# Performance work log

Hardware: AMD Instinct MI355X
Metric: run time of the kernel (lower is better)

## Reference

```python
import jax, jax.numpy as jnp
import numpy as np
from jax.scipy.special import logsumexp

V, C, S, H = 32000, 4096, 32, 512
B, T = 32, 256
NEG = jnp.float32(-1e10)  # masked_fill value used by mask_emission


def _res(x, w1, b1, w2, b2):
    # ResidualLayerOld: relu(lin1(x)); relu(lin2(h) + x)
    h = jax.nn.relu(x @ w1.T + b1)
    return jax.nn.relu(h @ w2.T + b2 + x)


def setup_inputs() -> dict:
    key = jax.random.key(0)
    ks = jax.random.split(key, 16)
    g = lambda i, shape, s=0.02: jax.random.normal(ks[i], shape, jnp.float32) * s
    return {
        "text": jax.random.randint(ks[0], (B, T), 0, V),
        "word2state": jax.random.randint(ks[1], (V, S), 0, C - 1),
        "start_emb": g(2, (C, H), 1.0),
        "start_w1": g(3, (H, H)), "start_b1": jnp.zeros((H,), jnp.float32),
        "start_w2": g(4, (H, H)), "start_b2": jnp.zeros((H,), jnp.float32),
        "start_w3": g(5, (1, H)), "start_b3": jnp.zeros((1,), jnp.float32),
        "state_emb": g(6, (C, H), 1.0),
        "trans_w1": g(7, (H, H)), "trans_b1": jnp.zeros((H,), jnp.float32),
        "trans_w2": g(8, (H, H)), "trans_b2": jnp.zeros((H,), jnp.float32),
        "next_state_proj": g(9, (C, H)),
        "preterminal_emb": g(10, (C, H), 1.0),
        "term_w1": g(11, (H, H)), "term_b1": jnp.zeros((H,), jnp.float32),
        "term_w2": g(12, (H, H)), "term_b2": jnp.zeros((H,), jnp.float32),
        "term_w3": g(13, (V, H)), "term_b3": jnp.zeros((V,), jnp.float32),
    }


def _forward(text, word2state, start_emb, start_w1, start_b1, start_w2, start_b2,
             start_w3, start_b3, state_emb, trans_w1, trans_b1, trans_w2, trans_b2,
             next_state_proj, preterminal_emb, term_w1, term_b1, term_w2, term_b2,
             term_w3, term_b3):
    ninf = -jnp.inf
    # start distribution over states [C]
    start = jax.nn.log_softmax(
        (_res(start_emb, start_w1, start_b1, start_w2, start_b2) @ start_w3.T + start_b3)[:, 0])
    # transition [C, C]: mask last column, row-normalize, mask last row (pad state)
    tl = _res(state_emb, trans_w1, trans_b1, trans_w2, trans_b2) @ next_state_proj.T
    tl = tl.at[:, -1].set(ninf)
    trans = jax.nn.log_softmax(tl, axis=-1)
    trans = jnp.where(jnp.isnan(trans), ninf, trans)
    trans = trans.at[-1, :].set(ninf)
    # emission [C, V]: sparse word2state mask, normalize over vocab
    el = _res(preterminal_emb, term_w1, term_b1, term_w2, term_b2) @ term_w3.T + term_b3
    emask = jnp.zeros((C, V), bool).at[
        word2state.reshape(-1), jnp.repeat(jnp.arange(V), S)].set(True)
    emit = jax.nn.log_softmax(jnp.where(emask, el, NEG), axis=-1)
    emit = jnp.where(jnp.isnan(emit), ninf, emit)
    emit = emit.at[-1, :].set(ninf)
    # clamp to the S states allowed for each observed word
    cs = word2state[text]                                  # [B, T, S]
    pot = trans[cs[:, :-1, :, None], cs[:, 1:, None, :]]   # [B, T-1, S, S] (cur, next)
    obs = emit[cs, text[:, :, None]]                       # [B, T, S]
    init = start[cs[:, 0]]                                 # [B, S]
    pot = pot + obs[:, 1:, None, :]                        # obs at t+1 on next axis
    pot = pot.at[:, 0].add(init[:, :, None] + obs[:, 0, :, None])
    pot = jnp.swapaxes(pot, -1, -2)                        # [B, T-1, next, prev]
    # log-domain forward scan (the fb kernel's alpha recursion)
    alpha0 = logsumexp(pot[:, 0], axis=-1)                 # [B, S]
    def step(alpha, p):
        return logsumexp(p + alpha[:, None, :], axis=-1), None
    alpha, _ = jax.lax.scan(step, alpha0, jnp.swapaxes(pot[:, 1:], 0, 1))
    return logsumexp(alpha, axis=-1).sum()                 # evidence (sum over batch)


def reference(text, word2state, start_emb, start_w1, start_b1, start_w2, start_b2,
              start_w3, start_b3, state_emb, trans_w1, trans_b1, trans_w2, trans_b2,
              next_state_proj, preterminal_emb, term_w1, term_b1, term_w2, term_b2,
              term_w3, term_b3):
    return _forward(text, word2state, start_emb, start_w1, start_b1, start_w2,
                    start_b2, start_w3, start_b3, state_emb, trans_w1, trans_b1,
                    trans_w2, trans_b2, next_state_proj, preterminal_emb, term_w1,
                    term_b1, term_w2, term_b2, term_w3, term_b3)
```

## Files before the change

### kernel.cpp

```cpp
#include <hip/hip_runtime.h>
#include <hip/hip_bf16.h>
#include <math.h>

#define NV 32000
#define NC 4096
#define NS 32
#define NH 512
#define NB 32
#define NT 256

typedef short s16x8 __attribute__((ext_vector_type(8)));
typedef float f32x4 __attribute__((ext_vector_type(4)));

__device__ __forceinline__ float wredMax(float v){
  #pragma unroll
  for (int o = 32; o; o >>= 1) v = fmaxf(v, __shfl_xor(v, o, 64));
  return v;
}
__device__ __forceinline__ float wredSum(float v){
  #pragma unroll
  for (int o = 32; o; o >>= 1) v += __shfl_xor(v, o, 64);
  return v;
}
__device__ __forceinline__ int f2ord(float f){ int i = __float_as_int(f); return i >= 0 ? i : (i ^ 0x7fffffff); }
__device__ __forceinline__ float ord2f(int i){ return __int_as_float(i >= 0 ? i : (i ^ 0x7fffffff)); }

__device__ __forceinline__ unsigned short f2bf(float x){
  unsigned int u = __float_as_uint(x);
  return (unsigned short)((u + 0x7fffu + ((u >> 16) & 1u)) >> 16);
}
__device__ __forceinline__ float bf2f(unsigned short h){
  return __uint_as_float((unsigned int)h << 16);
}

__device__ __forceinline__ void conv_body(const float* __restrict__ src,
                                          unsigned short* __restrict__ dst, int idx)
{
  const float* s = src + (size_t)idx * 8;
  float4 f0 = *(const float4*)s;
  float4 f1 = *(const float4*)(s + 4);
  float fv[8] = {f0.x, f0.y, f0.z, f0.w, f1.x, f1.y, f1.z, f1.w};
  s16x8 vh, vl;
  #pragma unroll
  for (int e = 0; e < 8; ++e) {
    unsigned short h = f2bf(fv[e]);
    vh[e] = (short)h;
    vl[e] = (short)f2bf(fv[e] - bf2f(h));
  }
  int r = idx >> 6, c8 = idx & 63;
  unsigned short* d = dst + (size_t)r * 1024 + c8 * 8;
  *(s16x8*)d = vh;
  *(s16x8*)(d + 512) = vl;
}

struct ConvArgs {
  const float* src[10];
  unsigned short* dst[10];
  int rows[10];
};

__global__ __launch_bounds__(256)
void conv_batch(ConvArgs a)
{
  int z = blockIdx.y;
  int idx = blockIdx.x * 256 + threadIdx.x;
  if (idx >= a.rows[z] * 64) return;
  conv_body(a.src[z], a.dst[z], idx);
}

template<int BM>
__global__ __launch_bounds__(256)
void gemm_bf16s(const unsigned short* __restrict__ Asp, const unsigned short* __restrict__ Bsp,
                float* __restrict__ Co, int M, int N, int K)
{
  constexpr int BN = 128;
  constexpr int MF = BM / 32;
  constexpr int NFR = 4;
  __shared__ char smem[BM * 128 + BN * 128];
  char* smA = smem;
  char* smB = smem + BM * 128;

  const int tid  = threadIdx.x;
  const int lane = tid & 63, w = tid >> 6;
  const int wr = w >> 1, wc = w & 1;
  const int bm = blockIdx.y * BM, bn = blockIdx.x * BN;
  const int lda = 2 * K;
  const int l8 = lane >> 3, s8 = lane & 7;
  const int frow = lane & 15, kgrp = lane >> 4;

  f32x4 acc[MF][NFR] = {};

  #pragma unroll 1
  for (int seg = 0; seg < 3; ++seg) {
    const int aoff = (seg == 1) ? K : 0;
    const int boff = (seg == 2) ? K : 0;
    #pragma unroll 1
    for (int k0 = 0; k0 < K; k0 += 64) {
      #pragma unroll
      for (int c = 0; c < MF; ++c) {
        int q = w * MF + c;
        int row = q * 8 + l8;
        s16x8 v = *(const s16x8*)(Asp + (size_t)(bm + row) * lda + aoff + k0 + s8 * 8);
        unsigned int o = (unsigned int)(row * 128 + (s8 << 4));
        o ^= (unsigned int)((row & 7) << 4);
        *(s16x8*)(smA + o) = v;
      }
      #pragma unroll
      for (int c = 0; c < NFR; ++c) {
        int q = w * NFR + c;
        int row = q * 8 + l8;
        s16x8 v = *(const s16x8*)(Bsp + (size_t)(bn + row) * lda + boff + k0 + s8 * 8);
        unsigned int o = (unsigned int)(row * 128 + (s8 << 4));
        o ^= (unsigned int)((row & 7) << 4);
        *(s16x8*)(smB + o) = v;
      }
      __syncthreads();
      #pragma unroll
      for (int kk = 0; kk < 64; kk += 32) {
        s16x8 af[MF], bfr[NFR];
        #pragma unroll
        for (int im = 0; im < MF; ++im) {
          int ar = wr * (BM / 2) + im * 16 + frow;
          unsigned int o = ((unsigned int)(ar * 128 + (kk + kgrp * 8) * 2)) ^ ((unsigned int)((ar & 7) << 4));
          af[im] = *(const s16x8*)(smA + o);
        }
        #pragma unroll
        for (int jn = 0; jn < NFR; ++jn) {
          int bc = wc * 64 + jn * 16 + frow;
          unsigned int o = ((unsigned int)(bc * 128 + (kk + kgrp * 8) * 2)) ^ ((unsigned int)((bc & 7) << 4));
          bfr[jn] = *(const s16x8*)(smB + o);
        }
        #pragma unroll
        for (int im = 0; im < MF; ++im)
          #pragma unroll
          for (int jn = 0; jn < NFR; ++jn)
            asm volatile("v_mfma_f32_16x16x32_bf16 %0, %1, %2, %0"
                         : "+v"(acc[im][jn]) : "v"(af[im]), "v"(bfr[jn]));
      }
      __syncthreads();
    }
  }
  asm volatile("s_nop 7\n\ts_nop 7" ::: );
  #pragma unroll
  for (int im = 0; im < MF; ++im) {
    int row0 = bm + wr * (BM / 2) + im * 16 + kgrp * 4;
    #pragma unroll
    for (int jn = 0; jn < NFR; ++jn) {
      int col = bn + wc * 64 + jn * 16 + frow;
      #pragma unroll
      for (int j = 0; j < 4; ++j)
        Co[(size_t)(row0 + j) * N + col] = acc[im][jn][j];
    }
  }
}

struct G3 {
  const unsigned short* A[3];
  const unsigned short* B[3];
  const float* bias[3];
  const float* res[3];
  float* Cf[3];
  unsigned short* Cs[3];
};

template<bool RES>
__global__ __launch_bounds__(256)
void gemm3(G3 a)
{
  constexpr int BM = 64, BN = 128, K = 512, N = 512;
  constexpr int MF = 2, NFR = 4;
  __shared__ char smem[BM * 128 + BN * 128];
  char* smA = smem;
  char* smB = smem + BM * 128;

  const int z = blockIdx.z;
  const unsigned short* Asp = a.A[z];
  const unsigned short* Bsp = a.B[z];
  const float* bias = a.bias[z];
  float* Cf = a.Cf[z];
  unsigned short* Cs = a.Cs[z];

  const int tid  = threadIdx.x;
  const int lane = tid & 63, w = tid >> 6;
  const int wr = w >> 1, wc = w & 1;
  const int bm = blockIdx.y * BM, bn = blockIdx.x * BN;
  const int lda = 2 * K;
  const int l8 = lane >> 3, s8 = lane & 7;
  const int frow = lane & 15, kgrp = lane >> 4;

  f32x4 acc[MF][NFR] = {};

  #pragma unroll 1
  for (int seg = 0; seg < 3; ++seg) {
    const int aoff = (seg == 1) ? K : 0;
    const int boff = (seg == 2) ? K : 0;
    #pragma unroll 1
    for (int k0 = 0; k0 < K; k0 += 64) {
      #pragma unroll
      for (int c = 0; c < MF; ++c) {
        int q = w * MF + c;
        int row = q * 8 + l8;
        s16x8 v = *(const s16x8*)(Asp + (size_t)(bm + row) * lda + aoff + k0 + s8 * 8);
        unsigned int o = (unsigned int)(row * 128 + (s8 << 4));
        o ^= (unsigned int)((row & 7) << 4);
        *(s16x8*)(smA + o) = v;
      }
      #pragma unroll
      for (int c = 0; c < NFR; ++c) {
        int q = w * NFR + c;
        int row = q * 8 + l8;
        s16x8 v = *(const s16x8*)(Bsp + (size_t)(bn + row) * lda + boff + k0 + s8 * 8);
        unsigned int o = (unsigned int)(row * 128 + (s8 << 4));
        o ^= (unsigned int)((row & 7) << 4);
        *(s16x8*)(smB + o) = v;
      }
      __syncthreads();
      #pragma unroll
      for (int kk = 0; kk < 64; kk += 32) {
        s16x8 af[MF], bfr[NFR];
        #pragma unroll
        for (int im = 0; im < MF; ++im) {
          int ar = wr * (BM / 2) + im * 16 + frow;
          unsigned int o = ((unsigned int)(ar * 128 + (kk + kgrp * 8) * 2)) ^ ((unsigned int)((ar & 7) << 4));
          af[im] = *(const s16x8*)(smA + o);
        }
        #pragma unroll
        for (int jn = 0; jn < NFR; ++jn) {
          int bc = wc * 64 + jn * 16 + frow;
          unsigned int o = ((unsigned int)(bc * 128 + (kk + kgrp * 8) * 2)) ^ ((unsigned int)((bc & 7) << 4));
          bfr[jn] = *(const s16x8*)(smB + o);
        }
        #pragma unroll
        for (int im = 0; im < MF; ++im)
          #pragma unroll
          for (int jn = 0; jn < NFR; ++jn)
            asm volatile("v_mfma_f32_16x16x32_bf16 %0, %1, %2, %0"
                         : "+v"(acc[im][jn]) : "v"(af[im]), "v"(bfr[jn]));
      }
      __syncthreads();
    }
  }
  asm volatile("s_nop 7\n\ts_nop 7" ::: );
  #pragma unroll
  for (int im = 0; im < MF; ++im) {
    int row0 = bm + wr * (BM / 2) + im * 16 + kgrp * 4;
    #pragma unroll
    for (int jn = 0; jn < NFR; ++jn) {
      int col = bn + wc * 64 + jn * 16 + frow;
      #pragma unroll
      for (int j = 0; j < 4; ++j) {
        int r = row0 + j;
        float v = acc[im][jn][j] + bias[col];
        if constexpr (RES) v += a.res[z][(size_t)r * N + col];
        v = fmaxf(v, 0.f);
        if (Cf) Cf[(size_t)r * N + col] = v;
        if (Cs) {
          unsigned short hi = f2bf(v);
          Cs[(size_t)r * 1024 + col] = hi;
          Cs[(size_t)r * 1024 + 512 + col] = f2bf(v - bf2f(hi));
        }
      }
    }
  }
}

__global__ __launch_bounds__(64)
void dot_head(const float* __restrict__ hS, const float* __restrict__ w3,
              const float* __restrict__ b3, float* __restrict__ sv)
{
  int c = blockIdx.x, lane = threadIdx.x;
  const float* hrow = hS + (size_t)c * NH;
  float acc = 0.f;
  #pragma unroll
  for (int e = 0; e < 8; ++e) acc += hrow[lane + e*64] * w3[lane + e*64];
  acc = wredSum(acc);
  if (lane == 0) sv[c] = acc + b3[0];
}

__global__ __launch_bounds__(1024)
void lse_vec(const float* __restrict__ x, int n, float* __restrict__ out)
{
  int tid = threadIdx.x;
  __shared__ float sm[16], ss[16];
  float m = -INFINITY;
  for (int i = tid; i < n; i += 1024) m = fmaxf(m, x[i]);
  m = wredMax(m);
  if ((tid & 63) == 0) sm[tid >> 6] = m;
  __syncthreads();
  m = sm[0];
  #pragma unroll
  for (int wv = 1; wv < 16; ++wv) m = fmaxf(m, sm[wv]);
  float s = 0.f;
  for (int i = tid; i < n; i += 1024) s += expf(x[i] - m);
  s = wredSum(s);
  if ((tid & 63) == 0) ss[tid >> 6] = s;
  __syncthreads();
  if (tid == 0) {
    float tot = 0.f;
    #pragma unroll
    for (int wv = 0; wv < 16; ++wv) tot += ss[wv];
    out[0] = m + logf(tot);
  }
}

__global__ __launch_bounds__(256)
void row_lse_trans(const float* __restrict__ tl, float* __restrict__ lse_t)
{
  int c = blockIdx.x;
  const float* row = tl + (size_t)c * NC;
  int tid = threadIdx.x;
  __shared__ float sm[4], ss[4];
  float m = -INFINITY;
  for (int n = tid; n < NC - 1; n += 256) m = fmaxf(m, row[n]);
  m = wredMax(m);
  if ((tid & 63) == 0) sm[tid >> 6] = m;
  __syncthreads();
  m = fmaxf(fmaxf(sm[0], sm[1]), fmaxf(sm[2], sm[3]));
  float s = 0.f;
  for (int n = tid; n < NC - 1; n += 256) s += expf(row[n] - m);
  s = wredSum(s);
  if ((tid & 63) == 0) ss[tid >> 6] = s;
  __syncthreads();
  if (tid == 0) lse_t[c] = m + logf(ss[0] + ss[1] + ss[2] + ss[3]);
}

__global__ __launch_bounds__(256)
void el_kernel(const int* __restrict__ w2s, const float* __restrict__ hP,
               const float* __restrict__ w3, const float* __restrict__ b3,
               float* __restrict__ el_g, unsigned int* __restrict__ vmask)
{
  int v = blockIdx.x;
  __shared__ float w3v[NH];
  __shared__ int crow[NS];
  int tid = threadIdx.x;
  if (tid < NS) crow[tid] = w2s[(size_t)v * NS + tid];
  for (int e = tid; e < NH; e += 256) w3v[e] = w3[(size_t)v * NH + e];
  __syncthreads();
  if (tid < 64) {
    bool valid = false;
    if (tid < NS) {
      valid = true;
      int c = crow[tid];
      for (int s2 = 0; s2 < tid; ++s2) if (crow[s2] == c) { valid = false; break; }
    }
    unsigned long long bal = __ballot(valid);
    if (tid == 0) vmask[v] = (unsigned int)(bal & 0xffffffffull);
  }
  int wave = tid >> 6, lane = tid & 63;
  float b3v = b3[v];
  #pragma unroll
  for (int q = 0; q < 8; ++q) {
    int s = wave * 8 + q;
    int c = crow[s];
    const float* hrow = hP + (size_t)c * NH;
    float acc = 0.f;
    #pragma unroll
    for (int e = 0; e < 8; ++e) acc += hrow[lane + e*64] * w3v[lane + e*64];
    acc = wredSum(acc);
    if (lane == 0) el_g[(size_t)v * NS + s] = acc + b3v;
  }
}

__global__ __launch_bounds__(256)
void init_e(int* __restrict__ emax, unsigned long long* __restrict__ esum)
{
  int i = blockIdx.x * 256 + threadIdx.x;
  if (i < NC) { emax[i] = 0x80000000; esum[i] = 0ull; }
}
__global__ __launch_bounds__(256)
void emit_max_k(const int* __restrict__ w2s, const float* __restrict__ el_g,
                const unsigned int* __restrict__ vmask, int* __restrict__ emax)
{
  int idx = blockIdx.x * 256 + threadIdx.x;
  int v = idx >> 5, s = idx & 31;
  if (!((vmask[v] >> s) & 1u)) return;
  atomicMax(&emax[w2s[idx]], f2ord(el_g[idx]));
}
__global__ __launch_bounds__(256)
void emit_sum_k(const int* __restrict__ w2s, const float* __restrict__ el_g,
                const unsigned int* __restrict__ vmask, const int* __restrict__ emax,
                unsigned long long* __restrict__ esum)
{
  int idx = blockIdx.x * 256 + threadIdx.x;
  int v = idx >> 5, s = idx & 31;
  if (!((vmask[v] >> s) & 1u)) return;
  int c = w2s[idx];
  float p = expf(el_g[idx] - ord2f(emax[c]));
  atomicAdd(&esum[c], (unsigned long long)(p * 0x1p40f));
}
__global__ __launch_bounds__(256)
void emit_fin_k(const int* __restrict__ emax, const unsigned long long* __restrict__ esum,
                float* __restrict__ lse_e)
{
  int c = blockIdx.x * 256 + threadIdx.x;
  if (c < NC) lse_e[c] = ord2f(emax[c]) + logf((float)esum[c] * 0x1p-40f);
}

__global__ __launch_bounds__(256)
void build_D(const int* __restrict__ text, const int* __restrict__ w2s,
             const float* __restrict__ el_g, const float* __restrict__ lse_e,
             const float* __restrict__ lse_t, const float* __restrict__ sv,
             const float* __restrict__ lse_s,
             float* __restrict__ Dall, float* __restrict__ Dlast,
             float* __restrict__ beta0, unsigned short* __restrict__ cs_all)
{
  int idx = blockIdx.x * 256 + threadIdx.x;
  int s = idx & 31;
  int bt = idx >> 5;
  int t = bt & (NT - 1);
  int b = bt >> 8;
  int v = text[bt];
  int c = w2s[(size_t)v * NS + s];
  cs_all[idx] = (unsigned short)c;
  float D = el_g[(size_t)v * NS + s] - lse_e[c] - lse_t[c];
  Dall[idx] = D;
  if (t == NT - 1) Dlast[b * NS + s] = D + lse_t[c];
  if (t == 0)      beta0[b * NS + s] = sv[c] - lse_s[0] + D;
}

__global__ __launch_bounds__(1024)
void gather_pot(const unsigned short* __restrict__ cs_all, const float* __restrict__ tl,
                float* __restrict__ pot)
{
  int t = blockIdx.x;
  int b = blockIdx.y;
  int tid = threadIdx.x;
  __shared__ unsigned short c1s[NS], c2s[NS];
  if (tid < NS) c1s[tid] = cs_all[((size_t)b * NT + t) * NS + tid];
  else if (tid < 2 * NS) c2s[tid - NS] = cs_all[((size_t)b * NT + t + 1) * NS + (tid - NS)];
  __syncthreads();
  int gi = tid >> 5, gj = tid & 31;
  float v = tl[(size_t)c1s[gi] * NC + c2s[gj]];
  pot[((size_t)b * (NT - 1) + t) * 1024 + gj * 32 + gi] = v;
}

__device__ __forceinline__ float lse_step(float4 p0, float4 p1, float4 p2, float4 p3,
                                          float beta, int h16)
{
  float pv[16] = {p0.x,p0.y,p0.z,p0.w, p1.x,p1.y,p1.z,p1.w,
                  p2.x,p2.y,p2.z,p2.w, p3.x,p3.y,p3.z,p3.w};
  float xs[16];
  #pragma unroll
  for (int q = 0; q < 16; ++q)
    xs[q] = pv[q] + __shfl(beta, h16 + q, 64);
  float a[8];
  #pragma unroll
  for (int q = 0; q < 8; ++q) a[q] = fmaxf(xs[q], xs[q + 8]);
  float c4[4];
  #pragma unroll
  for (int q = 0; q < 4; ++q) c4[q] = fmaxf(a[q], a[q + 4]);
  float m = fmaxf(fmaxf(c4[0], c4[1]), fmaxf(c4[2], c4[3]));
  m = fmaxf(m, __shfl_xor(m, 32, 64));
  float e[8];
  #pragma unroll
  for (int q = 0; q < 8; ++q) e[q] = __expf(xs[q] - m) + __expf(xs[q + 8] - m);
  float s4[4];
  #pragma unroll
  for (int q = 0; q < 4; ++q) s4[q] = e[q] + e[q + 4];
  float st = (s4[0] + s4[1]) + (s4[2] + s4[3]);
  st += __shfl_xor(st, 32, 64);
  return m + __logf(st);
}

__global__ __launch_bounds__(64)
void scan_kernel(const float* __restrict__ pot, const float* __restrict__ Dall,
                 const float* __restrict__ Dlast, const float* __restrict__ beta0,
                 float* __restrict__ out_b)
{
  const int b = blockIdx.x;
  const int lane = threadIdx.x;
  const int j = lane & 31;
  const int h16 = (lane >> 5) * 16;
  const float* potb = pot + (size_t)b * (NT - 1) * 1024 + j * 32 + h16;
  const float* Db = Dall + (size_t)b * NT * NS + j;

  float beta = beta0[b * NS + j];

  float4 A0 = *(const float4*)(potb + 0);
  float4 A1 = *(const float4*)(potb + 4);
  float4 A2 = *(const float4*)(potb + 8);
  float4 A3 = *(const float4*)(potb + 12);
  const float* pB0 = potb + 1024;
  float4 B0 = *(const float4*)(pB0 + 0);
  float4 B1 = *(const float4*)(pB0 + 4);
  float4 B2 = *(const float4*)(pB0 + 8);
  float4 B3 = *(const float4*)(pB0 + 12);
  float dA = Db[1 * NS];
  float dB = Db[2 * NS];

  #pragma unroll 1
  for (int t = 0; t < NT - 2; t += 2) {
    float r = lse_step(A0, A1, A2, A3, beta, h16);
    beta = r + dA;
    const float* pn = potb + (size_t)(t + 2) * 1024;
    A0 = *(const float4*)(pn + 0);
    A1 = *(const float4*)(pn + 4);
    A2 = *(const float4*)(pn + 8);
    A3 = *(const float4*)(pn + 12);
    dA = Db[(t + 3 < NT ? t + 3 : NT - 1) * NS];
    float r2 = lse_step(B0, B1, B2, B3, beta, h16);
    beta = r2 + dB;
    int tb = (t + 3 < NT - 1) ? t + 3 : NT - 2;
    const float* pn2 = potb + (size_t)tb * 1024;
    B0 = *(const float4*)(pn2 + 0);
    B1 = *(const float4*)(pn2 + 4);
    B2 = *(const float4*)(pn2 + 8);
    B3 = *(const float4*)(pn2 + 12);
    dB = Db[(t + 4 < NT ? t + 4 : NT - 1) * NS];
  }
  float r = lse_step(A0, A1, A2, A3, beta, h16);
  float rfin = r + Dlast[b * NS + j];

  float m = rfin;
  #pragma unroll
  for (int o = 16; o; o >>= 1) m = fmaxf(m, __shfl_xor(m, o, 32));
  float p = expf(rfin - m);
  #pragma unroll
  for (int o = 16; o; o >>= 1) p += __shfl_xor(p, o, 32);
  if (lane == 0) out_b[b] = m + logf(p);
}

__global__ void final_sum(const float* __restrict__ out_b, float* __restrict__ out)
{
  if (threadIdx.x == 0) {
    float s = 0.f;
    for (int b = 0; b < NB; ++b) s += out_b[b];
    out[0] = s;
  }
}

extern "C" void kernel_launch(void* const* d_in, const int* in_sizes, int n_in,
                              void* d_out, int out_size, void* d_ws, size_t ws_size,
                              hipStream_t stream)
{
  (void)in_sizes; (void)n_in; (void)out_size; (void)ws_size;
  const int*   text      = (const int*)d_in[0];
  const int*   w2s       = (const int*)d_in[1];
  const float* start_emb = (const float*)d_in[2];
  const float* start_w1  = (const float*)d_in[3];
  const float* start_b1  = (const float*)d_in[4];
  const float* start_w2  = (const float*)d_in[5];
  const float* start_b2  = (const float*)d_in[6];
  const float* start_w3  = (const float*)d_in[7];
  const float* start_b3  = (const float*)d_in[8];
  const float* state_emb = (const float*)d_in[9];
  const float* trans_w1  = (const float*)d_in[10];
  const float* trans_b1  = (const float*)d_in[11];
  const float* trans_w2  = (const float*)d_in[12];
  const float* trans_b2  = (const float*)d_in[13];
  const float* nsp       = (const float*)d_in[14];
  const float* pre_emb   = (const float*)d_in[15];
  const float* term_w1   = (const float*)d_in[16];
  const float* term_b1   = (const float*)d_in[17];
  const float* term_w2   = (const float*)d_in[18];
  const float* term_b2   = (const float*)d_in[19];
  const float* term_w3   = (const float*)d_in[20];
  const float* term_b3   = (const float*)d_in[21];

  float* tl    = (float*)d_ws;
  float* el_g  = tl + 16777216;
  float* sv    = el_g + 1024000;
  float* lse_t = sv + 4096;
  float* lse_e = lse_t + 4096;
  float* lse_s = lse_e + 4096;
  float* out_b = lse_s + 64;
  float* Dlast = out_b + 64;
  float* beta0 = Dlast + 1024;
  unsigned int* vmask = (unsigned int*)(beta0 + 1024);
  int* emax = (int*)(vmask + 32768);
  unsigned long long* esum = (unsigned long long*)(emax + 4096);
  unsigned short* sE_s  = (unsigned short*)(esum + 4096);
  unsigned short* tE_s  = sE_s  + 4194304;
  unsigned short* pE_s  = tE_s  + 4194304;
  unsigned short* nsp_s = pE_s  + 4194304;
  unsigned short* w1S_s = nsp_s + 4194304;
  unsigned short* w2S_s = w1S_s + 524288;
  unsigned short* w1T_s = w2S_s + 524288;
  unsigned short* w2T_s = w1T_s + 524288;
  unsigned short* w1P_s = w2T_s + 524288;
  unsigned short* w2P_s = w1P_s + 524288;
  unsigned short* h1s0  = w2P_s + 524288;
  unsigned short* h1s1  = h1s0 + 4194304;
  unsigned short* h1s2  = h1s1 + 4194304;
  float* h2f0 = (float*)sE_s;
  unsigned short* h2s1 = tE_s;
  float* h2f2 = (float*)pE_s;
  float* pot  = (float*)sE_s;
  float* Dall = (float*)h1s0;
  unsigned short* cs_all = (unsigned short*)((char*)h1s0 + 1048576);

  ConvArgs ca;
  ca.src[0]=start_emb; ca.dst[0]=sE_s;  ca.rows[0]=NC;
  ca.src[1]=state_emb; ca.dst[1]=tE_s;  ca.rows[1]=NC;
  ca.src[2]=pre_emb;   ca.dst[2]=pE_s;  ca.rows[2]=NC;
  ca.src[3]=nsp;       ca.dst[3]=nsp_s; ca.rows[3]=NC;
  ca.src[4]=start_w1;  ca.dst[4]=w1S_s; ca.rows[4]=NH;
  ca.src[5]=start_w2;  ca.dst[5]=w2S_s; ca.rows[5]=NH;
  ca.src[6]=trans_w1;  ca.dst[6]=w1T_s; ca.rows[6]=NH;
  ca.src[7]=trans_w2;  ca.dst[7]=w2T_s; ca.rows[7]=NH;
  ca.src[8]=term_w1;   ca.dst[8]=w1P_s; ca.rows[8]=NH;
  ca.src[9]=term_w2;   ca.dst[9]=w2P_s; ca.rows[9]=NH;
  conv_batch<<<dim3(1024, 10), 256, 0, stream>>>(ca);

  G3 g1;
  g1.A[0]=sE_s;  g1.A[1]=tE_s;  g1.A[2]=pE_s;
  g1.B[0]=w1S_s; g1.B[1]=w1T_s; g1.B[2]=w1P_s;
  g1.bias[0]=start_b1; g1.bias[1]=trans_b1; g1.bias[2]=term_b1;
  g1.res[0]=nullptr; g1.res[1]=nullptr; g1.res[2]=nullptr;
  g1.Cf[0]=nullptr; g1.Cf[1]=nullptr; g1.Cf[2]=nullptr;
  g1.Cs[0]=h1s0; g1.Cs[1]=h1s1; g1.Cs[2]=h1s2;
  gemm3<false><<<dim3(4, 64, 3), 256, 0, stream>>>(g1);

  G3 g2;
  g2.A[0]=h1s0;  g2.A[1]=h1s1;  g2.A[2]=h1s2;
  g2.B[0]=w2S_s; g2.B[1]=w2T_s; g2.B[2]=w2P_s;
  g2.bias[0]=start_b2; g2.bias[1]=trans_b2; g2.bias[2]=term_b2;
  g2.res[0]=start_emb; g2.res[1]=state_emb; g2.res[2]=pre_emb;
  g2.Cf[0]=h2f0; g2.Cf[1]=nullptr; g2.Cf[2]=h2f2;
  g2.Cs[0]=nullptr; g2.Cs[1]=h2s1; g2.Cs[2]=nullptr;
  gemm3<true><<<dim3(4, 64, 3), 256, 0, stream>>>(g2);

  dot_head<<<NC, 64, 0, stream>>>(h2f0, start_w3, start_b3, sv);
  lse_vec<<<1, 1024, 0, stream>>>(sv, NC, lse_s);

  gemm_bf16s<128><<<dim3(32, 32), 256, 0, stream>>>(h2s1, nsp_s, tl, NC, NC, NH);
  row_lse_trans<<<NC, 256, 0, stream>>>(tl, lse_t);

  el_kernel<<<NV, 256, 0, stream>>>(w2s, h2f2, term_w3, term_b3, el_g, vmask);
  init_e<<<16, 256, 0, stream>>>(emax, esum);
  emit_max_k<<<NV * NS / 256, 256, 0, stream>>>(w2s, el_g, vmask, emax);
  emit_sum_k<<<NV * NS / 256, 256, 0, stream>>>(w2s, el_g, vmask, emax, esum);
  emit_fin_k<<<NC / 256, 256, 0, stream>>>(emax, esum, lse_e);

  build_D<<<NB * NT * NS / 256, 256, 0, stream>>>(text, w2s, el_g, lse_e, lse_t, sv, lse_s,
                                                  Dall, Dlast, beta0, cs_all);
  gather_pot<<<dim3(NT - 1, NB), 1024, 0, stream>>>(cs_all, tl, pot);

  scan_kernel<<<NB, 64, 0, stream>>>(pot, Dall, Dlast, beta0, out_b);
  final_sum<<<1, 64, 0, stream>>>(out_b, (float*)d_out);
}
```

Before: 899.1 us.

## Fuse emission max into el kernel, split by state range, swizzle transition GEMM

The emission-logit kernel now runs as two passes, each restricted to half of the state range, so the gathered hidden rows of each pass are more likely to stay in cache. Each pass also performs the per-state atomicMax directly, which removes the separate emit_max kernel. The transition GEMM becomes a fixed-size kernel with a 1D grid and a block swizzle for L2 locality. row_lse_trans loads each row as float4s kept in registers, so the row is read once instead of twice. In exchange, the term_w3 weight matrix is now read by both passes, and the kernel launch order is rearranged.

```diff
diff --git a/kernel.cpp b/kernel.cpp
--- a/kernel.cpp
+++ b/kernel.cpp
@@ -68,22 +68,23 @@
   conv_body(a.src[z], a.dst[z], idx);
 }
 
-template<int BM>
-__global__ __launch_bounds__(256)
-void gemm_bf16s(const unsigned short* __restrict__ Asp, const unsigned short* __restrict__ Bsp,
-                float* __restrict__ Co, int M, int N, int K)
-{
-  constexpr int BN = 128;
-  constexpr int MF = BM / 32;
-  constexpr int NFR = 4;
+__global__ __launch_bounds__(256)
+void gemm_cc(const unsigned short* __restrict__ Asp, const unsigned short* __restrict__ Bsp,
+             float* __restrict__ Co)
+{
+  constexpr int BM = 128, BN = 128, K = NH, N = NC;
+  constexpr int MF = 4, NFR = 4;
   __shared__ char smem[BM * 128 + BN * 128];
   char* smA = smem;
   char* smB = smem + BM * 128;
 
+  const int bid = blockIdx.x;
+  const int swz = (bid & 7) * 128 + (bid >> 3);
+  const int bm = (swz >> 5) * BM, bn = (swz & 31) * BN;
+
   const int tid  = threadIdx.x;
   const int lane = tid & 63, w = tid >> 6;
   const int wr = w >> 1, wc = w & 1;
-  const int bm = blockIdx.y * BM, bn = blockIdx.x * BN;
   const int lda = 2 * K;
   const int l8 = lane >> 3, s8 = lane & 7;
   const int frow = lane & 15, kgrp = lane >> 4;
@@ -310,25 +311,40 @@
   const float* row = tl + (size_t)c * NC;
   int tid = threadIdx.x;
   __shared__ float sm[4], ss[4];
+  float4 vals[4];
   float m = -INFINITY;
-  for (int n = tid; n < NC - 1; n += 256) m = fmaxf(m, row[n]);
+  #pragma unroll
+  for (int r = 0; r < 4; ++r) {
+    int base = tid * 4 + r * 1024;
+    float4 vv = *(const float4*)(row + base);
+    if (base + 3 == NC - 1) vv.w = -INFINITY;
+    vals[r] = vv;
+    m = fmaxf(m, fmaxf(fmaxf(vv.x, vv.y), fmaxf(vv.z, vv.w)));
+  }
   m = wredMax(m);
   if ((tid & 63) == 0) sm[tid >> 6] = m;
   __syncthreads();
   m = fmaxf(fmaxf(sm[0], sm[1]), fmaxf(sm[2], sm[3]));
   float s = 0.f;
-  for (int n = tid; n < NC - 1; n += 256) s += expf(row[n] - m);
+  #pragma unroll
+  for (int r = 0; r < 4; ++r) {
+    float4 vv = vals[r];
+    s += expf(vv.x - m) + expf(vv.y - m) + expf(vv.z - m) + expf(vv.w - m);
+  }
   s = wredSum(s);
   if ((tid & 63) == 0) ss[tid >> 6] = s;
   __syncthreads();
   if (tid == 0) lse_t[c] = m + logf(ss[0] + ss[1] + ss[2] + ss[3]);
 }
 
-__global__ __launch_bounds__(256)
-void el_kernel(const int* __restrict__ w2s, const float* __restrict__ hP,
-               const float* __restrict__ w3, const float* __restrict__ b3,
-               float* __restrict__ el_g, unsigned int* __restrict__ vmask)
-{
+template<int PASS>
+__global__ __launch_bounds__(256)
+void el_chunk(const int* __restrict__ w2s, const float* __restrict__ hP,
+              const float* __restrict__ w3, const float* __restrict__ b3,
+              float* __restrict__ el_g, unsigned int* __restrict__ vmask,
+              int* __restrict__ emax)
+{
+  constexpr int C0 = PASS * (NC / 2), C1 = C0 + (NC / 2);
   int v = blockIdx.x;
   __shared__ float w3v[NH];
   __shared__ int crow[NS];
@@ -336,7 +352,7 @@
   if (tid < NS) crow[tid] = w2s[(size_t)v * NS + tid];
   for (int e = tid; e < NH; e += 256) w3v[e] = w3[(size_t)v * NH + e];
   __syncthreads();
-  if (tid < 64) {
+  if (PASS == 0 && tid < 64) {
     bool valid = false;
     if (tid < NS) {
       valid = true;
@@ -352,12 +368,17 @@
   for (int q = 0; q < 8; ++q) {
     int s = wave * 8 + q;
     int c = crow[s];
+    if (c < C0 || c >= C1) continue;
     const float* hrow = hP + (size_t)c * NH;
     float acc = 0.f;
     #pragma unroll
     for (int e = 0; e < 8; ++e) acc += hrow[lane + e*64] * w3v[lane + e*64];
     acc = wredSum(acc);
-    if (lane == 0) el_g[(size_t)v * NS + s] = acc + b3v;
+    if (lane == 0) {
+      float val = acc + b3v;
+      el_g[(size_t)v * NS + s] = val;
+      atomicMax(&emax[c], f2ord(val));
+    }
   }
 }
 
@@ -366,15 +387,6 @@
 {
   int i = blockIdx.x * 256 + threadIdx.x;
   if (i < NC) { emax[i] = 0x80000000; esum[i] = 0ull; }
-}
-__global__ __launch_bounds__(256)
-void emit_max_k(const int* __restrict__ w2s, const float* __restrict__ el_g,
-                const unsigned int* __restrict__ vmask, int* __restrict__ emax)
-{
-  int idx = blockIdx.x * 256 + threadIdx.x;
-  int v = idx >> 5, s = idx & 31;
-  if (!((vmask[v] >> s) & 1u)) return;
-  atomicMax(&emax[w2s[idx]], f2ord(el_g[idx]));
 }
 __global__ __launch_bounds__(256)
 void emit_sum_k(const int* __restrict__ w2s, const float* __restrict__ el_g,
@@ -623,14 +635,14 @@
   dot_head<<<NC, 64, 0, stream>>>(h2f0, start_w3, start_b3, sv);
   lse_vec<<<1, 1024, 0, stream>>>(sv, NC, lse_s);
 
-  gemm_bf16s<128><<<dim3(32, 32), 256, 0, stream>>>(h2s1, nsp_s, tl, NC, NC, NH);
-  row_lse_trans<<<NC, 256, 0, stream>>>(tl, lse_t);
-
-  el_kernel<<<NV, 256, 0, stream>>>(w2s, h2f2, term_w3, term_b3, el_g, vmask);
   init_e<<<16, 256, 0, stream>>>(emax, esum);
-  emit_max_k<<<NV * NS / 256, 256, 0, stream>>>(w2s, el_g, vmask, emax);
+  el_chunk<0><<<NV, 256, 0, stream>>>(w2s, h2f2, term_w3, term_b3, el_g, vmask, emax);
+  el_chunk<1><<<NV, 256, 0, stream>>>(w2s, h2f2, term_w3, term_b3, el_g, vmask, emax);
   emit_sum_k<<<NV * NS / 256, 256, 0, stream>>>(w2s, el_g, vmask, emax, esum);
   emit_fin_k<<<NC / 256, 256, 0, stream>>>(emax, esum, lse_e);
+
+  gemm_cc<<<1024, 256, 0, stream>>>(h2s1, nsp_s, tl);
+  row_lse_trans<<<NC, 256, 0, stream>>>(tl, lse_t);
 
   build_D<<<NB * NT * NS / 256, 256, 0, stream>>>(text, w2s, el_g, lse_e, lse_t, sv, lse_s,
                                                   Dall, Dlast, beta0, cs_all);
```

Result: faster. 879.3 us (-2.2%).
